# Performance work log

Measured on AMD Instinct MI355X. Metric: run time of the kernel, lower is better.

Reference implementation:

```python
import jax, jax.numpy as jnp
import numpy as np

INPUT_DIM, DK, DV = 1024, 128, 128


def setup_inputs() -> dict:
    key = jax.random.key(0)
    ks = jax.random.split(key, 7)
    s = 0.02
    return {
        "x": jax.random.normal(ks[0], (4, 4096, INPUT_DIM), dtype=jnp.float32),
        "Wq": jax.random.normal(ks[1], (INPUT_DIM, DK), dtype=jnp.float32) * s,
        "bq": jnp.zeros((DK,), dtype=jnp.float32),
        "Wk": jax.random.normal(ks[2], (INPUT_DIM, DK), dtype=jnp.float32) * s,
        "bk": jnp.zeros((DK,), dtype=jnp.float32),
        "Wv": jax.random.normal(ks[3], (INPUT_DIM, DV), dtype=jnp.float32) * s,
        "bv": jnp.zeros((DV,), dtype=jnp.float32),
    }


def reference(x, Wq, bq, Wk, bk, Wv, bv):
    # single-head self-attention with explicit QK^T softmax V
    scale = DK ** (-0.5)
    q = x @ Wq + bq          # [b, s, dk]
    k = x @ Wk + bk          # [b, s, dk]
    v = x @ Wv + bv          # [b, s, dv]
    scores = jnp.einsum("bqd,bkd->bqk", q, k) * scale  # [b, s, s]
    attn = jax.nn.softmax(scores, axis=-1)
    return jnp.einsum("bqk,bkd->bqd", attn, v)  # [b, s, dv]
```

## Files before the change

kernel.cpp:

```cpp
#include <hip/hip_runtime.h>
#include <hip/hip_bf16.h>
#include <math.h>
#include <stdint.h>


#define SM_SCALE2 0.1275310225216245f

using f32x4  = __attribute__((ext_vector_type(4))) float;
using f32x16 = __attribute__((ext_vector_type(16))) float;
using bf16x8 = __attribute__((ext_vector_type(8))) short;
using s16x4  = __attribute__((ext_vector_type(4))) short;

#define GLD16(gp, lp) __builtin_amdgcn_global_load_lds(                      \
    (const __attribute__((address_space(1))) void*)(gp),                     \
    (__attribute__((address_space(3))) void*)(lp), 16, 0, 0)

__device__ __forceinline__ short f2bf(float f) {
  union { __hip_bfloat16 h; short s; } u;
  u.h = __float2bfloat16(f);
  return u.s;
}

__global__ __launch_bounds__(256) void wprep_k(const float* __restrict__ Wq,
                                               const float* __restrict__ Wk,
                                               const float* __restrict__ Wv,
                                               short* __restrict__ Wt) {
  int tid = blockIdx.x * 256 + threadIdx.x;
  int mat = tid >> 17;
  int r   = tid & 131071;
  int k   = r >> 7;
  int col = r & 127;
  const float* W = (mat == 0) ? Wq : ((mat == 1) ? Wk : Wv);
  Wt[mat * 131072 + col * 1024 + k] = f2bf(W[k * 128 + col]);
}

__global__ __launch_bounds__(256) void proj_k(const float* __restrict__ x,
                                              const short* __restrict__ Wt,
                                              const float* __restrict__ bq,
                                              const float* __restrict__ bk,
                                              const float* __restrict__ bv,
                                              short* __restrict__ Qb,
                                              short* __restrict__ Kb,
                                              short* __restrict__ Vt) {
  const int mat = blockIdx.y;
  const int r0  = blockIdx.x * 64;
  const int tid  = threadIdx.x;
  const int lane = tid & 63;
  const int w    = tid >> 6;
  const int g    = lane >> 4;
  const int l15  = lane & 15;

  __shared__ __align__(16) char smem[8192 + 16384];
  short* xs = (short*)smem;
  char*  wt = smem + 8192;

  const char* Wtm = (const char*)(Wt + mat * 131072);

  f32x4 acc[8];
  #pragma unroll
  for (int i = 0; i < 8; ++i) acc[i] = (f32x4){0.f, 0.f, 0.f, 0.f};

  for (int kt = 0; kt < 16; ++kt) {
    __syncthreads();
    {
      const int row = tid >> 2;
      #pragma unroll
      for (int p = 0; p < 4; ++p) {
        const int s = (tid & 3) + 4 * p;
        const float4 v = *(const float4*)(x + (size_t)(r0 + row) * 1024 + kt * 64 + s * 4);
        s16x4 h = { f2bf(v.x), f2bf(v.y), f2bf(v.z), f2bf(v.w) };
        *(s16x4*)((char*)xs + row * 128 + (((s >> 1) ^ (row & 7)) << 4) + ((s & 1) << 3)) = h;
      }
    }
    #pragma unroll
    for (int c = 0; c < 4; ++c) {
      const int o  = w * 4096 + c * 1024 + lane * 16;
      const int cr = o >> 7;
      const int cb = (o >> 4) & 7;
      GLD16(Wtm + (size_t)cr * 2048 + kt * 128 + ((cb ^ (cr & 7)) << 4),
            wt + w * 4096 + c * 1024);
    }
    __syncthreads();
    #pragma unroll
    for (int kc = 0; kc < 2; ++kc) {
      const int arow = w * 16 + l15;
      bf16x8 a = *(const bf16x8*)((char*)xs + arow * 128 +
                                  ((((kc << 2) + g) ^ (l15 & 7)) << 4));
      #pragma unroll
      for (int cb = 0; cb < 8; ++cb) {
        const int brow = (cb << 4) + l15;
        bf16x8 b = *(const bf16x8*)(wt + brow * 128 +
                                    ((((kc << 2) + g) ^ (l15 & 7)) << 4));
        acc[cb] = __builtin_amdgcn_mfma_f32_16x16x32_bf16(a, b, acc[cb], 0, 0, 0);
      }
    }
  }

  const float* bias = (mat == 0) ? bq : ((mat == 1) ? bk : bv);
  #pragma unroll
  for (int cb = 0; cb < 8; ++cb) {
    const float bc = bias[(cb << 4) + l15];
    #pragma unroll
    for (int r = 0; r < 4; ++r) acc[cb][r] += bc;
  }

  if (mat < 2) {
    short* dst = (mat == 0) ? Qb : Kb;
    #pragma unroll
    for (int cb = 0; cb < 8; ++cb)
      #pragma unroll
      for (int r = 0; r < 4; ++r)
        dst[(size_t)(r0 + w * 16 + (g << 2) + r) * 128 + (cb << 4) + l15] =
            f2bf(acc[cb][r]);
  } else {
    __syncthreads();
    short* tb = (short*)smem;
    #pragma unroll
    for (int cb = 0; cb < 8; ++cb)
      #pragma unroll
      for (int r = 0; r < 4; ++r)
        tb[((cb << 4) + l15) * 72 + w * 16 + (g << 2) + r] = f2bf(acc[cb][r]);
    __syncthreads();
    const int bb = r0 >> 12;
    const int s0 = r0 & 4095;
    const int d  = tid >> 1;
    #pragma unroll
    for (int j = 0; j < 4; ++j) {
      uint4 vd = *(const uint4*)((char*)tb + d * 144 + (tid & 1) * 64 + j * 16);
      *(uint4*)((char*)Vt +
                ((size_t)(bb * 128 + d) * 4096 + s0 + (tid & 1) * 32 + j * 8) * 2) = vd;
    }
  }
}

__global__ __launch_bounds__(256, 2) void attn_part_k(
    const short* __restrict__ Qb, const short* __restrict__ Kb,
    const short* __restrict__ Vt, float* __restrict__ part,
    float2* __restrict__ ml, float* __restrict__ out, int ns, int direct) {
  const int nwg  = gridDim.x;
  const int bid  = blockIdx.x;
  const int orig = (bid & 7) * (nwg >> 3) + (bid >> 3);
  const int split = orig >> 7;
  const int qb    = orig & 127;
  const int nkt   = 64 / ns;
  const int kt0   = split * nkt;

  const int tid  = threadIdx.x;
  const int lane = tid & 63;
  const int w    = tid >> 6;
  const int l31  = lane & 31;
  const bool hi  = lane >= 32;

  __shared__ __align__(16) char smem[65536];

  const int bb = qb >> 5;
  const size_t qg = (size_t)qb * 128 + w * 32 + l31;

  const char* Kg = (const char*)(Kb + ((size_t)bb << 19));
  const char* Vg = (const char*)(Vt + ((size_t)bb << 19));

  bf16x8 qf[8];
  {
    const short* qp = Qb + qg * 128;
    #pragma unroll
    for (int kd = 0; kd < 8; ++kd)
      qf[kd] = *(const bf16x8*)(qp + 16 * kd + (hi ? 8 : 0));
  }

  float m = -__builtin_inff(), lsum = 0.f;
  f32x16 oacc[4];
  #pragma unroll
  for (int dt = 0; dt < 4; ++dt) oacc[dt] = (f32x16)(0.0f);

#define STAGE(BUF, KT) do {                                                   \
    char* kb_ = smem + (BUF) * 32768;                                         \
    char* vb_ = kb_ + 16384;                                                  \
    _Pragma("unroll")                                                         \
    for (int c = 0; c < 4; ++c) {                                             \
      const int o   = w * 4096 + c * 1024 + lane * 16;                        \
      const int kr  = o >> 8;                                                 \
      const int kc_ = (o >> 4) & 15;                                          \
      GLD16(Kg + (size_t)((KT) * 64 + kr) * 256 + ((kc_ ^ (kr & 15)) << 4),   \
            kb_ + w * 4096 + c * 1024);                                       \
      const int dr  = o >> 7;                                                 \
      const int dc_ = (o >> 4) & 7;                                           \
      GLD16(Vg + (size_t)dr * 8192 + (size_t)(KT) * 128 + ((dc_ ^ (dr & 7)) << 4), \
            vb_ + w * 4096 + c * 1024);                                       \
    }                                                                         \
  } while (0)

  STAGE(0, kt0);
  __syncthreads();

  for (int t = 0; t < nkt; ++t) {
    const int cur = t & 1;
    if (t + 1 < nkt) STAGE(cur ^ 1, kt0 + t + 1);

    const char* KT_ = smem + cur * 32768;
    const char* VT_ = KT_ + 16384;

    f32x16 s0 = (f32x16)(0.0f), s1 = (f32x16)(0.0f);
    #pragma unroll
    for (int kd = 0; kd < 8; ++kd) {
      const int ch = (((2 * kd + (hi ? 1 : 0)) ^ (l31 & 15)) << 4);
      bf16x8 k0 = *(const bf16x8*)(KT_ + l31 * 256 + ch);
      bf16x8 k1 = *(const bf16x8*)(KT_ + (32 + l31) * 256 + ch);
      s0 = __builtin_amdgcn_mfma_f32_32x32x16_bf16(k0, qf[kd], s0, 0, 0, 0);
      s1 = __builtin_amdgcn_mfma_f32_32x32x16_bf16(k1, qf[kd], s1, 0, 0, 0);
    }

    float mx = s0[0];
    #pragma unroll
    for (int i = 1; i < 16; ++i) mx = fmaxf(mx, s0[i]);
    #pragma unroll
    for (int i = 0; i < 16; ++i) mx = fmaxf(mx, s1[i]);
    mx = fmaxf(mx, __shfl_xor(mx, 32));
    mx *= SM_SCALE2;
    if (!__all(mx - m <= 8.f)) {
      const float mn = fmaxf(m, mx);
      const float al = exp2f(m - mn);
      m = mn;
      lsum *= al;
      #pragma unroll
      for (int dt = 0; dt < 4; ++dt)
        #pragma unroll
        for (int i = 0; i < 16; ++i) oacc[dt][i] *= al;
    }
    float rs = 0.f;
    #pragma unroll
    for (int i = 0; i < 16; ++i) { s0[i] = exp2f(fmaf(s0[i], SM_SCALE2, -m)); rs += s0[i]; }
    #pragma unroll
    for (int i = 0; i < 16; ++i) { s1[i] = exp2f(fmaf(s1[i], SM_SCALE2, -m)); rs += s1[i]; }
    rs += __shfl_xor(rs, 32);
    lsum += rs;

    unsigned int W[2][4][2];
    #pragma unroll
    for (int rho = 0; rho < 4; ++rho)
      #pragma unroll
      for (int rh = 0; rh < 2; ++rh) {
        asm("v_cvt_pk_bf16_f32 %0, %1, %2"
            : "=v"(W[0][rho][rh]) : "v"(s0[4 * rho + 2 * rh]), "v"(s0[4 * rho + 2 * rh + 1]));
        asm("v_cvt_pk_bf16_f32 %0, %1, %2"
            : "=v"(W[1][rho][rh]) : "v"(s1[4 * rho + 2 * rh]), "v"(s1[4 * rho + 2 * rh + 1]));
      }

    #pragma unroll
    for (int ks = 0; ks < 4; ++ks) {
      const int t2 = ks >> 1, ksl = ks & 1;
      const unsigned int wl0 = W[t2][2 * ksl][0],     wl1 = W[t2][2 * ksl][1];
      const unsigned int wh0 = W[t2][2 * ksl + 1][0], wh1 = W[t2][2 * ksl + 1][1];
      const unsigned int r0 = __shfl_xor(hi ? wl0 : wh0, 32);
      const unsigned int r1 = __shfl_xor(hi ? wl1 : wh1, 32);
      union { unsigned int u[4]; bf16x8 v; } pb;
      pb.u[0] = hi ? r0 : wl0;
      pb.u[1] = hi ? r1 : wl1;
      pb.u[2] = hi ? wh0 : r0;
      pb.u[3] = hi ? wh1 : r1;
      #pragma unroll
      for (int dt = 0; dt < 4; ++dt) {
        const int row = 32 * dt + l31;
        bf16x8 vf = *(const bf16x8*)(VT_ + row * 128 +
                                     (((2 * ks + (hi ? 1 : 0)) ^ (row & 7)) << 4));
        oacc[dt] = __builtin_amdgcn_mfma_f32_32x32x16_bf16(vf, pb.v, oacc[dt], 0, 0, 0);
      }
    }

    __syncthreads();
  }
#undef STAGE

  const float sc = direct ? (1.f / lsum) : 1.f;
  float* dst = direct ? (out + qg * 128)
                      : (part + ((size_t)split * 16384 + qg) * 128);
  #pragma unroll
  for (int dt = 0; dt < 4; ++dt)
    #pragma unroll
    for (int rq = 0; rq < 4; ++rq) {
      f32x4 v = { oacc[dt][4 * rq + 0] * sc, oacc[dt][4 * rq + 1] * sc,
                  oacc[dt][4 * rq + 2] * sc, oacc[dt][4 * rq + 3] * sc };
      *(f32x4*)(dst + dt * 32 + rq * 8 + (hi ? 4 : 0)) = v;
    }
  if (!direct && lane < 32)
    ml[(size_t)split * 16384 + qg] = make_float2(m, lsum);
}

__global__ __launch_bounds__(256) void merge_k(const float* __restrict__ part,
                                               const float2* __restrict__ ml,
                                               float* __restrict__ out, int ns) {
  const int idx = blockIdx.x * 256 + threadIdx.x;
  const int row = idx >> 5;
  const int c4  = idx & 31;

  float M = -__builtin_inff();
  for (int s = 0; s < ns; ++s) M = fmaxf(M, ml[s * 16384 + row].x);
  float L = 0.f;
  for (int s = 0; s < ns; ++s) {
    const float2 v = ml[s * 16384 + row];
    L += v.y * exp2f(v.x - M);
  }
  const float invL = 1.f / L;

  f32x4 o = (f32x4){0.f, 0.f, 0.f, 0.f};
  for (int s = 0; s < ns; ++s) {
    const float wgt = exp2f(ml[s * 16384 + row].x - M) * invL;
    const f32x4 a = *(const f32x4*)(part + ((size_t)s * 16384 + row) * 128 + c4 * 4);
    o += a * wgt;
  }
  *(f32x4*)(out + (size_t)row * 128 + c4 * 4) = o;
}

extern "C" void kernel_launch(void* const* d_in, const int* in_sizes, int n_in,
                              void* d_out, int out_size, void* d_ws, size_t ws_size,
                              hipStream_t stream) {
  (void)in_sizes; (void)n_in; (void)out_size;
  const float* x  = (const float*)d_in[0];
  const float* Wq = (const float*)d_in[1];
  const float* bq = (const float*)d_in[2];
  const float* Wk = (const float*)d_in[3];
  const float* bk = (const float*)d_in[4];
  const float* Wv = (const float*)d_in[5];
  const float* bv = (const float*)d_in[6];
  float* out = (float*)d_out;

  char* ws = (char*)d_ws;
  short* Wt = (short*)ws;
  short* Qb = (short*)(ws + 786432);
  short* Kb = (short*)(ws + 786432 + 4194304);
  short* Vt = (short*)(ws + 786432 + 2 * 4194304);
  const size_t base = 786432 + 3ull * 4194304;

  const size_t per_split = 16384ull * 128 * 4 + 16384ull * 8;
  int ns = 0;
  if (ws_size >= base + 4 * per_split)      ns = 4;
  else if (ws_size >= base + 2 * per_split) ns = 2;
  const int direct = (ns == 0);
  if (direct) ns = 1;

  float*  part = (float*)(ws + base);
  float2* mlp  = (float2*)(ws + base + (size_t)ns * 16384ull * 128 * 4);

  wprep_k<<<dim3(1536), dim3(256), 0, stream>>>(Wq, Wk, Wv, Wt);
  proj_k<<<dim3(256, 3), dim3(256), 0, stream>>>(x, Wt, bq, bk, bv, Qb, Kb, Vt);
  attn_part_k<<<dim3(128 * ns), dim3(256), 0, stream>>>(Qb, Kb, Vt, part, mlp, out,
                                                        ns, direct);
  if (!direct)
    merge_k<<<dim3(2048), dim3(256), 0, stream>>>(part, mlp, out, ns);
}
```

Baseline: 103.7 us.

## Fuse QKV projections, double-buffer proj, single-buffer V and allow eight splits

The projection kernel now computes Q, K and V in one block, reading each x tile once instead of three times. It double-buffers the x and weight tiles so that global loads overlap the MFMA work. The softmax scale is folded into Q at projection time, which removes a multiply per score in attention. Attention keeps K double-buffered but V single-buffered to cut LDS to 48KB and raise occupancy to three blocks per CU, and the host can pick eight KV splits. The costs are extra barriers, a serial V load after each tile, larger merge traffic and higher register pressure in proj.

Result: slower. 141.8 us (+36.8%).

```diff
diff --git a/kernel.cpp b/kernel.cpp
--- a/kernel.cpp
+++ b/kernel.cpp
@@ -42,7 +42,6 @@
                                               short* __restrict__ Qb,
                                               short* __restrict__ Kb,
                                               short* __restrict__ Vt) {
-  const int mat = blockIdx.y;
   const int r0  = blockIdx.x * 64;
   const int tid  = threadIdx.x;
   const int lane = tid & 63;
@@ -50,76 +49,129 @@
   const int g    = lane >> 4;
   const int l15  = lane & 15;
 
-  __shared__ __align__(16) char smem[8192 + 16384];
-  short* xs = (short*)smem;
-  char*  wt = smem + 8192;
-
-  const char* Wtm = (const char*)(Wt + mat * 131072);
-
-  f32x4 acc[8];
+  __shared__ __align__(16) char smem[114688];
+  const char* Wtb = (const char*)Wt;
+
+  f32x4 acc[3][4][2];
   #pragma unroll
-  for (int i = 0; i < 8; ++i) acc[i] = (f32x4){0.f, 0.f, 0.f, 0.f};
-
-  for (int kt = 0; kt < 16; ++kt) {
-    __syncthreads();
-    {
-      const int row = tid >> 2;
+  for (int m = 0; m < 3; ++m)
+    #pragma unroll
+    for (int rb = 0; rb < 4; ++rb)
+      #pragma unroll
+      for (int cb = 0; cb < 2; ++cb) acc[m][rb][cb] = (f32x4){0.f, 0.f, 0.f, 0.f};
+
+  const int xrow = tid >> 2;
+
+  {
+    char* xs0 = smem;
+    char* wt0 = smem + 16384;
+    #pragma unroll
+    for (int p = 0; p < 4; ++p) {
+      const int s = (tid & 3) + 4 * p;
+      const float4 v = *(const float4*)(x + (size_t)(r0 + xrow) * 1024 + s * 4);
+      s16x4 h = { f2bf(v.x), f2bf(v.y), f2bf(v.z), f2bf(v.w) };
+      *(s16x4*)(xs0 + xrow * 128 + (((s >> 1) ^ (xrow & 7)) << 4) + ((s & 1) << 3)) = h;
+    }
+    #pragma unroll
+    for (int m = 0; m < 3; ++m)
+      #pragma unroll
+      for (int c = 0; c < 4; ++c) {
+        const int om = w * 4096 + c * 1024 + lane * 16;
+        const int cr = om >> 7;
+        const int cb = (om >> 4) & 7;
+        GLD16(Wtb + m * 262144 + (size_t)cr * 2048 + ((cb ^ (cr & 7)) << 4),
+              wt0 + m * 16384 + w * 4096 + c * 1024);
+      }
+  }
+  __syncthreads();
+
+  for (int t = 0; t < 16; ++t) {
+    const int cur = t & 1;
+    float4 fx[4];
+    if (t < 15) {
       #pragma unroll
       for (int p = 0; p < 4; ++p) {
         const int s = (tid & 3) + 4 * p;
-        const float4 v = *(const float4*)(x + (size_t)(r0 + row) * 1024 + kt * 64 + s * 4);
-        s16x4 h = { f2bf(v.x), f2bf(v.y), f2bf(v.z), f2bf(v.w) };
-        *(s16x4*)((char*)xs + row * 128 + (((s >> 1) ^ (row & 7)) << 4) + ((s & 1) << 3)) = h;
+        fx[p] = *(const float4*)(x + (size_t)(r0 + xrow) * 1024 + (t + 1) * 64 + s * 4);
       }
-    }
-    #pragma unroll
-    for (int c = 0; c < 4; ++c) {
-      const int o  = w * 4096 + c * 1024 + lane * 16;
-      const int cr = o >> 7;
-      const int cb = (o >> 4) & 7;
-      GLD16(Wtm + (size_t)cr * 2048 + kt * 128 + ((cb ^ (cr & 7)) << 4),
-            wt + w * 4096 + c * 1024);
+      char* wtn = smem + 16384 + (cur ^ 1) * 49152;
+      #pragma unroll
+      for (int m = 0; m < 3; ++m)
+        #pragma unroll
+        for (int c = 0; c < 4; ++c) {
+          const int om = w * 4096 + c * 1024 + lane * 16;
+          const int cr = om >> 7;
+          const int cb = (om >> 4) & 7;
+          GLD16(Wtb + m * 262144 + (size_t)cr * 2048 + (t + 1) * 128 + ((cb ^ (cr & 7)) << 4),
+                wtn + m * 16384 + w * 4096 + c * 1024);
+        }
+    }
+
+    const char* xb = smem + cur * 8192;
+    const char* wb = smem + 16384 + cur * 49152;
+    #pragma unroll
+    for (int kc = 0; kc < 2; ++kc) {
+      bf16x8 a[4];
+      #pragma unroll
+      for (int rb = 0; rb < 4; ++rb)
+        a[rb] = *(const bf16x8*)(xb + (rb * 16 + l15) * 128 +
+                                 ((((kc << 2) + g) ^ (l15 & 7)) << 4));
+      #pragma unroll
+      for (int m = 0; m < 3; ++m)
+        #pragma unroll
+        for (int cb = 0; cb < 2; ++cb) {
+          const int col = w * 32 + cb * 16 + l15;
+          bf16x8 b = *(const bf16x8*)(wb + m * 16384 + col * 128 +
+                                      ((((kc << 2) + g) ^ (l15 & 7)) << 4));
+          #pragma unroll
+          for (int rb = 0; rb < 4; ++rb)
+            acc[m][rb][cb] = __builtin_amdgcn_mfma_f32_16x16x32_bf16(a[rb], b,
+                                                                     acc[m][rb][cb], 0, 0, 0);
+        }
+    }
+
+    if (t < 15) {
+      char* xsn = smem + (cur ^ 1) * 8192;
+      #pragma unroll
+      for (int p = 0; p < 4; ++p) {
+        const int s = (tid & 3) + 4 * p;
+        s16x4 h = { f2bf(fx[p].x), f2bf(fx[p].y), f2bf(fx[p].z), f2bf(fx[p].w) };
+        *(s16x4*)(xsn + xrow * 128 + (((s >> 1) ^ (xrow & 7)) << 4) + ((s & 1) << 3)) = h;
+      }
     }
     __syncthreads();
-    #pragma unroll
-    for (int kc = 0; kc < 2; ++kc) {
-      const int arow = w * 16 + l15;
-      bf16x8 a = *(const bf16x8*)((char*)xs + arow * 128 +
-                                  ((((kc << 2) + g) ^ (l15 & 7)) << 4));
-      #pragma unroll
-      for (int cb = 0; cb < 8; ++cb) {
-        const int brow = (cb << 4) + l15;
-        bf16x8 b = *(const bf16x8*)(wt + brow * 128 +
-                                    ((((kc << 2) + g) ^ (l15 & 7)) << 4));
-        acc[cb] = __builtin_amdgcn_mfma_f32_16x16x32_bf16(a, b, acc[cb], 0, 0, 0);
-      }
-    }
-  }
-
-  const float* bias = (mat == 0) ? bq : ((mat == 1) ? bk : bv);
+  }
+
   #pragma unroll
-  for (int cb = 0; cb < 8; ++cb) {
-    const float bc = bias[(cb << 4) + l15];
-    #pragma unroll
-    for (int r = 0; r < 4; ++r) acc[cb][r] += bc;
-  }
-
-  if (mat < 2) {
-    short* dst = (mat == 0) ? Qb : Kb;
-    #pragma unroll
-    for (int cb = 0; cb < 8; ++cb)
-      #pragma unroll
-      for (int r = 0; r < 4; ++r)
-        dst[(size_t)(r0 + w * 16 + (g << 2) + r) * 128 + (cb << 4) + l15] =
-            f2bf(acc[cb][r]);
-  } else {
-    __syncthreads();
+  for (int m = 0; m < 2; ++m) {
+    short* dst = (m == 0) ? Qb : Kb;
+    const float* bias = (m == 0) ? bq : bk;
+    #pragma unroll
+    for (int cb = 0; cb < 2; ++cb) {
+      const int col = w * 32 + cb * 16 + l15;
+      const float bc = bias[col];
+      #pragma unroll
+      for (int rb = 0; rb < 4; ++rb)
+        #pragma unroll
+        for (int r = 0; r < 4; ++r) {
+          float v = acc[m][rb][cb][r] + bc;
+          if (m == 0) v *= SM_SCALE2;
+          dst[(size_t)(r0 + rb * 16 + (g << 2) + r) * 128 + col] = f2bf(v);
+        }
+    }
+  }
+  {
     short* tb = (short*)smem;
     #pragma unroll
-    for (int cb = 0; cb < 8; ++cb)
-      #pragma unroll
-      for (int r = 0; r < 4; ++r)
-        tb[((cb << 4) + l15) * 72 + w * 16 + (g << 2) + r] = f2bf(acc[cb][r]);
+    for (int cb = 0; cb < 2; ++cb) {
+      const int col = w * 32 + cb * 16 + l15;
+      const float bc = bv[col];
+      #pragma unroll
+      for (int rb = 0; rb < 4; ++rb)
+        #pragma unroll
+        for (int r = 0; r < 4; ++r)
+          tb[col * 72 + rb * 16 + (g << 2) + r] = f2bf(acc[2][rb][cb][r] + bc);
+    }
     __syncthreads();
     const int bb = r0 >> 12;
     const int s0 = r0 & 4095;
@@ -133,7 +185,7 @@
   }
 }
 
-__global__ __launch_bounds__(256, 2) void attn_part_k(
+__global__ __launch_bounds__(256, 3) void attn_part_k(
     const short* __restrict__ Qb, const short* __restrict__ Kb,
     const short* __restrict__ Vt, float* __restrict__ part,
     float2* __restrict__ ml, float* __restrict__ out, int ns, int direct) {
@@ -151,7 +203,7 @@
   const int l31  = lane & 31;
   const bool hi  = lane >= 32;
 
-  __shared__ __align__(16) char smem[65536];
+  __shared__ __align__(16) char smem[49152];
 
   const int bb = qb >> 5;
   const size_t qg = (size_t)qb * 128 + w * 32 + l31;
@@ -172,9 +224,8 @@
   #pragma unroll
   for (int dt = 0; dt < 4; ++dt) oacc[dt] = (f32x16)(0.0f);
 
-#define STAGE(BUF, KT) do {                                                   \
-    char* kb_ = smem + (BUF) * 32768;                                         \
-    char* vb_ = kb_ + 16384;                                                  \
+#define STAGE_K(BUF, KT) do {                                                 \
+    char* kb_ = smem + (BUF) * 16384;                                         \
     _Pragma("unroll")                                                         \
     for (int c = 0; c < 4; ++c) {                                             \
       const int o   = w * 4096 + c * 1024 + lane * 16;                        \
@@ -182,6 +233,14 @@
       const int kc_ = (o >> 4) & 15;                                          \
       GLD16(Kg + (size_t)((KT) * 64 + kr) * 256 + ((kc_ ^ (kr & 15)) << 4),   \
             kb_ + w * 4096 + c * 1024);                                       \
+    }                                                                         \
+  } while (0)
+
+#define STAGE_V(KT) do {                                                      \
+    char* vb_ = smem + 32768;                                                 \
+    _Pragma("unroll")                                                         \
+    for (int c = 0; c < 4; ++c) {                                             \
+      const int o   = w * 4096 + c * 1024 + lane * 16;                        \
       const int dr  = o >> 7;                                                 \
       const int dc_ = (o >> 4) & 7;                                           \
       GLD16(Vg + (size_t)dr * 8192 + (size_t)(KT) * 128 + ((dc_ ^ (dr & 7)) << 4), \
@@ -189,15 +248,16 @@
     }                                                                         \
   } while (0)
 
-  STAGE(0, kt0);
+  STAGE_K(0, kt0);
+  STAGE_V(kt0);
   __syncthreads();
 
   for (int t = 0; t < nkt; ++t) {
     const int cur = t & 1;
-    if (t + 1 < nkt) STAGE(cur ^ 1, kt0 + t + 1);
-
-    const char* KT_ = smem + cur * 32768;
-    const char* VT_ = KT_ + 16384;
+    if (t + 1 < nkt) STAGE_K(cur ^ 1, kt0 + t + 1);
+
+    const char* KT_ = smem + cur * 16384;
+    const char* VT_ = smem + 32768;
 
     f32x16 s0 = (f32x16)(0.0f), s1 = (f32x16)(0.0f);
     #pragma unroll
@@ -215,7 +275,6 @@
     #pragma unroll
     for (int i = 0; i < 16; ++i) mx = fmaxf(mx, s1[i]);
     mx = fmaxf(mx, __shfl_xor(mx, 32));
-    mx *= SM_SCALE2;
     if (!__all(mx - m <= 8.f)) {
       const float mn = fmaxf(m, mx);
       const float al = exp2f(m - mn);
@@ -228,9 +287,9 @@
     }
     float rs = 0.f;
     #pragma unroll
-    for (int i = 0; i < 16; ++i) { s0[i] = exp2f(fmaf(s0[i], SM_SCALE2, -m)); rs += s0[i]; }
-    #pragma unroll
-    for (int i = 0; i < 16; ++i) { s1[i] = exp2f(fmaf(s1[i], SM_SCALE2, -m)); rs += s1[i]; }
+    for (int i = 0; i < 16; ++i) { s0[i] = exp2f(s0[i] - m); rs += s0[i]; }
+    #pragma unroll
+    for (int i = 0; i < 16; ++i) { s1[i] = exp2f(s1[i] - m); rs += s1[i]; }
     rs += __shfl_xor(rs, 32);
     lsum += rs;
 
@@ -244,6 +303,8 @@
         asm("v_cvt_pk_bf16_f32 %0, %1, %2"
             : "=v"(W[1][rho][rh]) : "v"(s1[4 * rho + 2 * rh]), "v"(s1[4 * rho + 2 * rh + 1]));
       }
+
+    __syncthreads();
 
     #pragma unroll
     for (int ks = 0; ks < 4; ++ks) {
@@ -267,8 +328,10 @@
     }
 
     __syncthreads();
-  }
-#undef STAGE
+    if (t + 1 < nkt) STAGE_V(kt0 + t + 1);
+  }
+#undef STAGE_K
+#undef STAGE_V
 
   const float sc = direct ? (1.f / lsum) : 1.f;
   float* dst = direct ? (out + qg * 128)
@@ -332,7 +395,8 @@
 
   const size_t per_split = 16384ull * 128 * 4 + 16384ull * 8;
   int ns = 0;
-  if (ws_size >= base + 4 * per_split)      ns = 4;
+  if (ws_size >= base + 8 * per_split)      ns = 8;
+  else if (ws_size >= base + 4 * per_split) ns = 4;
   else if (ws_size >= base + 2 * per_split) ns = 2;
   const int direct = (ns == 0);
   if (direct) ns = 1;
@@ -341,7 +405,7 @@
   float2* mlp  = (float2*)(ws + base + (size_t)ns * 16384ull * 128 * 4);
 
   wprep_k<<<dim3(1536), dim3(256), 0, stream>>>(Wq, Wk, Wv, Wt);
-  proj_k<<<dim3(256, 3), dim3(256), 0, stream>>>(x, Wt, bq, bk, bv, Qb, Kb, Vt);
+  proj_k<<<dim3(256), dim3(256), 0, stream>>>(x, Wt, bq, bk, bv, Qb, Kb, Vt);
   attn_part_k<<<dim3(128 * ns), dim3(256), 0, stream>>>(Qb, Kb, Vt, part, mlp, out,
                                                         ns, direct);
   if (!direct)
```
